# Kernel optimization log

Hardware: AMD Instinct MI355X
Metric: run time of the kernel (lower is better)

The kernel has to match this reference:

```python
import jax, jax.numpy as jnp
import numpy as np

N_EMBD = 2048
N_EXPERTS = 8
MOE_LOSS_COEFF = 0.01


def setup_inputs() -> dict:
    key = jax.random.key(0)
    kx, kw = jax.random.split(key)
    x = jax.random.normal(kx, (4, 4096, N_EMBD), dtype=jnp.float32)
    # nn.Linear(n_embd, n_experts, bias=False): weight [n_experts, n_embd]
    bound = 1.0 / np.sqrt(N_EMBD)
    W = jax.random.uniform(kw, (N_EXPERTS, N_EMBD), dtype=jnp.float32,
                           minval=-bound, maxval=bound)
    return {"x": x, "W": W}


def reference(x, W):
    n_experts = W.shape[0]
    # gate linear: logits [B, T, E]
    logits = jnp.einsum("btd,ed->bte", x, W)
    probs = jax.nn.softmax(logits, axis=-1)
    # top-2 selection and renormalization
    top2_vals, top2_idx = jax.lax.top_k(probs, 2)  # [B,T,2]
    gate_probs_top2 = top2_vals / jnp.sum(top2_vals, axis=-1, keepdims=True)
    # aux load-balancing loss stats
    importance = jnp.mean(probs, axis=(0, 1))  # [E]
    top1_idx = jnp.argmax(probs, axis=-1)      # [B,T]
    one_hot = jax.nn.one_hot(top1_idx, n_experts, dtype=jnp.float32)
    load = jnp.mean(one_hot, axis=(0, 1))      # [E]
    aux_loss = n_experts * jnp.sum(importance * load) * MOE_LOSS_COEFF
    return gate_probs_top2, top2_idx, aux_loss
```

## Files before the change

kernel.cpp:

```cpp
#include <hip/hip_runtime.h>

#define NEMBD 2048
#define ROW4 (NEMBD / 4)
#define HITERS (ROW4 / 32)

__global__ __launch_bounds__(256) void gate_kernel(
    const float* __restrict__ x, const float* __restrict__ W,
    float* __restrict__ out, float* __restrict__ ws, int ntok, int ngroups)
{
    const int tid  = threadIdx.x;
    const int lane = tid & 63;
    const int wid  = tid >> 6;
    const int half = lane >> 5;
    const int j    = lane & 31;
    const int nwaves = gridDim.x * 4;
    int gw = blockIdx.x * 4 + wid;

    const float4* X4 = (const float4*)x;
    const float4* W4 = (const float4*)W;
    float* out_p = out;
    float* out_i = out + 2 * ntok;

    float imp_acc = 0.f, load_acc = 0.f;

    for (int g = gw; g < ngroups; g += nwaves) {
        const int base = g * 8;
        const int tb = base + 4 * half;

        float a[32];
        #pragma unroll
        for (int q = 0; q < 32; ++q) a[q] = 0.f;

        for (int i = 0; i < HITERS; ++i) {
            const int col = i * 32 + j;
            float4 xv[4];
            #pragma unroll
            for (int k = 0; k < 4; ++k)
                xv[k] = X4[(tb + k) * ROW4 + col];
            #pragma unroll
            for (int e = 0; e < 8; ++e) {
                float4 wv = W4[e * ROW4 + col];
                #pragma unroll
                for (int k = 0; k < 4; ++k) {
                    a[k * 8 + e] += xv[k].x * wv.x + xv[k].y * wv.y
                                  + xv[k].z * wv.z + xv[k].w * wv.w;
                }
            }
        }

        #pragma unroll
        for (int s = 0; s < 5; ++s) {
            const int hm = 16 >> s;
            const bool hi = (lane & hm) != 0;
            #pragma unroll
            for (int q = 0; q < 16; ++q) {
                if (q < hm) {
                    float send = hi ? a[q] : a[q + hm];
                    float recv = __shfl_xor(send, hm, 64);
                    float keep = hi ? a[q + hm] : a[q];
                    a[q] = keep + recv;
                }
            }
        }
        const float logit = a[0];
        const int e = lane & 7;
        const int k = lane >> 3;
        const bool tvalid = (base + k) < ntok;

        float m = logit;
        #pragma unroll
        for (int mm = 1; mm <= 4; mm <<= 1) m = fmaxf(m, __shfl_xor(m, mm, 64));
        float p = __expf(logit - m);
        float ssum = p;
        #pragma unroll
        for (int mm = 1; mm <= 4; mm <<= 1) ssum += __shfl_xor(ssum, mm, 64);
        const float prob = p / ssum;

        float v1 = prob, v2 = -1.f;
        int   i1 = e,    i2 = -1;
        #pragma unroll
        for (int mm = 1; mm <= 4; mm <<= 1) {
            float b1 = __shfl_xor(v1, mm, 64);
            float b2 = __shfl_xor(v2, mm, 64);
            int  bi1 = __shfl_xor(i1, mm, 64);
            int  bi2 = __shfl_xor(i2, mm, 64);
            bool aw = (v1 > b1) || (v1 == b1 && i1 < bi1);
            float w1 = aw ? v1 : b1;  int wi1 = aw ? i1 : bi1;
            float l1 = aw ? b1 : v1;  int li1 = aw ? bi1 : i1;
            float w2 = aw ? v2 : b2;  int wi2 = aw ? i2 : bi2;
            bool sw = (l1 > w2) || (l1 == w2 && li1 < wi2);
            v1 = w1; i1 = wi1;
            v2 = sw ? l1 : w2;  i2 = sw ? li1 : wi2;
        }

        if (e == 0 && tvalid) {
            const int t = base + k;
            const float denom = v1 + v2;
            out_p[2 * t]     = v1 / denom;
            out_p[2 * t + 1] = v2 / denom;
            out_i[2 * t]     = (float)i1;
            out_i[2 * t + 1] = (float)i2;
        }

        float pc = tvalid ? prob : 0.f;
        float oc = (tvalid && e == i1) ? 1.f : 0.f;
        #pragma unroll
        for (int mm = 8; mm <= 32; mm <<= 1) {
            pc += __shfl_xor(pc, mm, 64);
            oc += __shfl_xor(oc, mm, 64);
        }
        imp_acc  += pc;
        load_acc += oc;
    }

    __shared__ float part[4][16];
    if (lane < 8) {
        part[wid][lane]     = imp_acc;
        part[wid][lane + 8] = load_acc;
    }
    __syncthreads();
    if (tid < 16) {
        ws[blockIdx.x * 16 + tid] =
            part[0][tid] + part[1][tid] + part[2][tid] + part[3][tid];
    }
}

__global__ void finalize_kernel(const float* __restrict__ ws,
                                float* __restrict__ out, int nblk, int ntok)
{
    __shared__ float s[16][16];
    __shared__ float tot[16];
    const int t = threadIdx.x;
    const int slot = t & 15, chunk = t >> 4;
    float p = 0.f;
    for (int b = chunk; b < nblk; b += 16) p += ws[b * 16 + slot];
    s[chunk][slot] = p;
    __syncthreads();
    if (t < 16) {
        float v = 0.f;
        #pragma unroll
        for (int c = 0; c < 16; ++c) v += s[c][t];
        tot[t] = v;
    }
    __syncthreads();
    if (t == 0) {
        const float inv = 1.f / (float)ntok;
        float aux = 0.f;
        #pragma unroll
        for (int e = 0; e < 8; ++e)
            aux += (tot[e] * inv) * (tot[8 + e] * inv);
        out[4 * ntok] = 8.f * aux * 0.01f;
    }
}

extern "C" void kernel_launch(void* const* d_in, const int* in_sizes, int n_in,
                              void* d_out, int out_size, void* d_ws, size_t ws_size,
                              hipStream_t stream)
{
    const float* x = (const float*)d_in[0];
    const float* W = (const float*)d_in[1];
    const int ntok    = in_sizes[0] / NEMBD;
    const int ngroups = (ntok + 7) / 8;
    const int nblocks = (ngroups + 3) / 4;

    gate_kernel<<<nblocks, 256, 0, stream>>>(
        x, W, (float*)d_out, (float*)d_ws, ntok, ngroups);
    finalize_kernel<<<1, 256, 0, stream>>>(
        (const float*)d_ws, (float*)d_out, nblocks, ntok);
}
```

Measured before the change: 238.8 us.

## Map two tokens per wave with full-row lanes and atomic aux-stat reduction

Each wave now handles two tokens, and all 64 lanes stride one full row, instead of eight tokens split across half-waves. This quadruples the block count, cuts the accumulator array from 32 to 16 registers and makes each token load a contiguous 1 KB segment. The per-block workspace plus multi-stage finalize reduction is replaced by atomicAdd into 16 global floats, zeroed by a memset. That adds an extra memset launch and atomic contention across 2048 blocks, and it makes float summation order nondeterministic.

After: 215.0 us. 10.0% less time.

```diff
diff --git a/kernel.cpp b/kernel.cpp
--- a/kernel.cpp
+++ b/kernel.cpp
@@ -2,153 +2,127 @@
 
 #define NEMBD 2048
 #define ROW4 (NEMBD / 4)
-#define HITERS (ROW4 / 32)
+#define CHUNKS (ROW4 / 64)
 
 __global__ __launch_bounds__(256) void gate_kernel(
     const float* __restrict__ x, const float* __restrict__ W,
-    float* __restrict__ out, float* __restrict__ ws, int ntok, int ngroups)
+    float* __restrict__ out, float* __restrict__ ws, int ntok)
 {
     const int tid  = threadIdx.x;
     const int lane = tid & 63;
     const int wid  = tid >> 6;
-    const int half = lane >> 5;
-    const int j    = lane & 31;
-    const int nwaves = gridDim.x * 4;
-    int gw = blockIdx.x * 4 + wid;
+
+    const int t0 = blockIdx.x * 8 + wid * 2;
+    const bool va0 = t0 < ntok, va1 = (t0 + 1) < ntok;
 
     const float4* X4 = (const float4*)x;
     const float4* W4 = (const float4*)W;
     float* out_p = out;
     float* out_i = out + 2 * ntok;
 
-    float imp_acc = 0.f, load_acc = 0.f;
+    float a[16];
+    #pragma unroll
+    for (int q = 0; q < 16; ++q) a[q] = 0.f;
 
-    for (int g = gw; g < ngroups; g += nwaves) {
-        const int base = g * 8;
-        const int tb = base + 4 * half;
+    const float4 z4 = make_float4(0.f, 0.f, 0.f, 0.f);
 
-        float a[32];
+    #pragma unroll 2
+    for (int i = 0; i < CHUNKS; ++i) {
+        const int col = i * 64 + lane;
+        float4 x0 = va0 ? X4[(size_t)t0 * ROW4 + col] : z4;
+        float4 x1 = va1 ? X4[(size_t)(t0 + 1) * ROW4 + col] : z4;
         #pragma unroll
-        for (int q = 0; q < 32; ++q) a[q] = 0.f;
+        for (int e = 0; e < 8; ++e) {
+            float4 wv = W4[e * ROW4 + col];
+            a[e]     += x0.x * wv.x + x0.y * wv.y + x0.z * wv.z + x0.w * wv.w;
+            a[8 + e] += x1.x * wv.x + x1.y * wv.y + x1.z * wv.z + x1.w * wv.w;
+        }
+    }
 
-        for (int i = 0; i < HITERS; ++i) {
-            const int col = i * 32 + j;
-            float4 xv[4];
-            #pragma unroll
-            for (int k = 0; k < 4; ++k)
-                xv[k] = X4[(tb + k) * ROW4 + col];
-            #pragma unroll
-            for (int e = 0; e < 8; ++e) {
-                float4 wv = W4[e * ROW4 + col];
-                #pragma unroll
-                for (int k = 0; k < 4; ++k) {
-                    a[k * 8 + e] += xv[k].x * wv.x + xv[k].y * wv.y
-                                  + xv[k].z * wv.z + xv[k].w * wv.w;
-                }
+    #pragma unroll
+    for (int q = 0; q < 16; ++q) a[q] += __shfl_xor(a[q], 32, 64);
+    #pragma unroll
+    for (int q = 0; q < 16; ++q) a[q] += __shfl_xor(a[q], 16, 64);
+    #pragma unroll
+    for (int s = 0; s < 4; ++s) {
+        const int hm = 8 >> s;
+        const bool hi = (lane & hm) != 0;
+        #pragma unroll
+        for (int q = 0; q < 8; ++q) {
+            if (q < hm) {
+                float send = hi ? a[q] : a[q + hm];
+                float recv = __shfl_xor(send, hm, 64);
+                float keep = hi ? a[q + hm] : a[q];
+                a[q] = keep + recv;
             }
         }
+    }
+    const float logit = a[0];
+    const int e = lane & 7;
+    const int k = (lane >> 3) & 1;
+    const bool tvalid = (t0 + k) < ntok;
 
-        #pragma unroll
-        for (int s = 0; s < 5; ++s) {
-            const int hm = 16 >> s;
-            const bool hi = (lane & hm) != 0;
-            #pragma unroll
-            for (int q = 0; q < 16; ++q) {
-                if (q < hm) {
-                    float send = hi ? a[q] : a[q + hm];
-                    float recv = __shfl_xor(send, hm, 64);
-                    float keep = hi ? a[q + hm] : a[q];
-                    a[q] = keep + recv;
-                }
-            }
-        }
-        const float logit = a[0];
-        const int e = lane & 7;
-        const int k = lane >> 3;
-        const bool tvalid = (base + k) < ntok;
+    float m = logit;
+    #pragma unroll
+    for (int mm = 1; mm <= 4; mm <<= 1) m = fmaxf(m, __shfl_xor(m, mm, 64));
+    float p = __expf(logit - m);
+    float ssum = p;
+    #pragma unroll
+    for (int mm = 1; mm <= 4; mm <<= 1) ssum += __shfl_xor(ssum, mm, 64);
+    const float prob = p / ssum;
 
-        float m = logit;
-        #pragma unroll
-        for (int mm = 1; mm <= 4; mm <<= 1) m = fmaxf(m, __shfl_xor(m, mm, 64));
-        float p = __expf(logit - m);
-        float ssum = p;
-        #pragma unroll
-        for (int mm = 1; mm <= 4; mm <<= 1) ssum += __shfl_xor(ssum, mm, 64);
-        const float prob = p / ssum;
+    float v1 = prob, v2 = -1.f;
+    int   i1 = e,    i2 = -1;
+    #pragma unroll
+    for (int mm = 1; mm <= 4; mm <<= 1) {
+        float b1 = __shfl_xor(v1, mm, 64);
+        float b2 = __shfl_xor(v2, mm, 64);
+        int  bi1 = __shfl_xor(i1, mm, 64);
+        int  bi2 = __shfl_xor(i2, mm, 64);
+        bool aw = (v1 > b1) || (v1 == b1 && i1 < bi1);
+        float w1 = aw ? v1 : b1;  int wi1 = aw ? i1 : bi1;
+        float l1 = aw ? b1 : v1;  int li1 = aw ? bi1 : i1;
+        float w2 = aw ? v2 : b2;  int wi2 = aw ? i2 : bi2;
+        bool sw = (l1 > w2) || (l1 == w2 && li1 < wi2);
+        v1 = w1; i1 = wi1;
+        v2 = sw ? l1 : w2;  i2 = sw ? li1 : wi2;
+    }
 
-        float v1 = prob, v2 = -1.f;
-        int   i1 = e,    i2 = -1;
-        #pragma unroll
-        for (int mm = 1; mm <= 4; mm <<= 1) {
-            float b1 = __shfl_xor(v1, mm, 64);
-            float b2 = __shfl_xor(v2, mm, 64);
-            int  bi1 = __shfl_xor(i1, mm, 64);
-            int  bi2 = __shfl_xor(i2, mm, 64);
-            bool aw = (v1 > b1) || (v1 == b1 && i1 < bi1);
-            float w1 = aw ? v1 : b1;  int wi1 = aw ? i1 : bi1;
-            float l1 = aw ? b1 : v1;  int li1 = aw ? bi1 : i1;
-            float w2 = aw ? v2 : b2;  int wi2 = aw ? i2 : bi2;
-            bool sw = (l1 > w2) || (l1 == w2 && li1 < wi2);
-            v1 = w1; i1 = wi1;
-            v2 = sw ? l1 : w2;  i2 = sw ? li1 : wi2;
-        }
+    if (e == 0 && lane < 16 && tvalid) {
+        const int t = t0 + k;
+        const float denom = v1 + v2;
+        out_p[2 * t]     = v1 / denom;
+        out_p[2 * t + 1] = v2 / denom;
+        out_i[2 * t]     = (float)i1;
+        out_i[2 * t + 1] = (float)i2;
+    }
 
-        if (e == 0 && tvalid) {
-            const int t = base + k;
-            const float denom = v1 + v2;
-            out_p[2 * t]     = v1 / denom;
-            out_p[2 * t + 1] = v2 / denom;
-            out_i[2 * t]     = (float)i1;
-            out_i[2 * t + 1] = (float)i2;
-        }
-
-        float pc = tvalid ? prob : 0.f;
-        float oc = (tvalid && e == i1) ? 1.f : 0.f;
-        #pragma unroll
-        for (int mm = 8; mm <= 32; mm <<= 1) {
-            pc += __shfl_xor(pc, mm, 64);
-            oc += __shfl_xor(oc, mm, 64);
-        }
-        imp_acc  += pc;
-        load_acc += oc;
-    }
+    float pc = tvalid ? prob : 0.f;
+    float oc = (tvalid && e == i1) ? 1.f : 0.f;
+    pc += __shfl_xor(pc, 8, 64);
+    oc += __shfl_xor(oc, 8, 64);
 
     __shared__ float part[4][16];
     if (lane < 8) {
-        part[wid][lane]     = imp_acc;
-        part[wid][lane + 8] = load_acc;
+        part[wid][lane]     = pc;
+        part[wid][lane + 8] = oc;
     }
     __syncthreads();
     if (tid < 16) {
-        ws[blockIdx.x * 16 + tid] =
-            part[0][tid] + part[1][tid] + part[2][tid] + part[3][tid];
+        atomicAdd(&ws[tid],
+                  part[0][tid] + part[1][tid] + part[2][tid] + part[3][tid]);
     }
 }
 
 __global__ void finalize_kernel(const float* __restrict__ ws,
-                                float* __restrict__ out, int nblk, int ntok)
+                                float* __restrict__ out, int ntok)
 {
-    __shared__ float s[16][16];
-    __shared__ float tot[16];
-    const int t = threadIdx.x;
-    const int slot = t & 15, chunk = t >> 4;
-    float p = 0.f;
-    for (int b = chunk; b < nblk; b += 16) p += ws[b * 16 + slot];
-    s[chunk][slot] = p;
-    __syncthreads();
-    if (t < 16) {
-        float v = 0.f;
-        #pragma unroll
-        for (int c = 0; c < 16; ++c) v += s[c][t];
-        tot[t] = v;
-    }
-    __syncthreads();
-    if (t == 0) {
+    if (threadIdx.x == 0) {
         const float inv = 1.f / (float)ntok;
         float aux = 0.f;
         #pragma unroll
         for (int e = 0; e < 8; ++e)
-            aux += (tot[e] * inv) * (tot[8 + e] * inv);
+            aux += (ws[e] * inv) * (ws[8 + e] * inv);
         out[4 * ntok] = 8.f * aux * 0.01f;
     }
 }
@@ -160,11 +134,11 @@
     const float* x = (const float*)d_in[0];
     const float* W = (const float*)d_in[1];
     const int ntok    = in_sizes[0] / NEMBD;
-    const int ngroups = (ntok + 7) / 8;
-    const int nblocks = (ngroups + 3) / 4;
+    const int nblocks = (ntok + 7) / 8;
 
+    hipMemsetAsync(d_ws, 0, 16 * sizeof(float), stream);
     gate_kernel<<<nblocks, 256, 0, stream>>>(
-        x, W, (float*)d_out, (float*)d_ws, ntok, ngroups);
-    finalize_kernel<<<1, 256, 0, stream>>>(
-        (const float*)d_ws, (float*)d_out, nblocks, ntok);
+        x, W, (float*)d_out, (float*)d_ws, ntok);
+    finalize_kernel<<<1, 64, 0, stream>>>(
+        (const float*)d_ws, (float*)d_out, ntok);
 }
```
